# Kernel optimization log

Hardware: AMD Instinct MI355X
Metric: run time of the kernel (lower is better)

Reference implementation:

```python
import jax, jax.numpy as jnp
import numpy as np

B, C, N = 8, 512, 2048
QK, V = 512, 512


def setup_inputs() -> dict:
    key = jax.random.key(0)
    k1, k2, k3, k4 = jax.random.split(key, 4)
    x = jax.random.normal(k1, (B, C, N), dtype=jnp.float32)
    # conv1x1 weights: [out_ch, in_ch]
    w_q = jax.random.normal(k2, (QK, C), dtype=jnp.float32) * (1.0 / np.sqrt(C))
    w_k = w_q  # torch init clones k into q; still independent params
    w_v = jax.random.normal(k3, (V, C), dtype=jnp.float32) * (1.0 / np.sqrt(C))
    b_v = jnp.zeros((V,), dtype=jnp.float32)
    return {"x": x, "w_q": w_q, "w_k": w_k, "w_v": w_v, "b_v": b_v}


def reference(x, w_q, w_k, w_v, b_v):
    temperature = jnp.asarray(w_q.shape[0], x.dtype) ** 0.5
    # conv1x1: [B,C,N] -> [B,out,N]
    q = jnp.einsum('qc,bcn->bnq', w_q, x)            # [B,N,QK]
    k = jnp.einsum('kc,bcn->bkn', w_k, x)            # [B,QK,N]
    v = jnp.einsum('vc,bcn->bnv', w_v, x) + b_v      # [B,N,V]
    energy = jnp.einsum('bnq,bqm->bnm', q, k) / temperature  # [B,N,N]
    attn = jax.nn.softmax(energy, axis=-1)
    out = jnp.einsum('bnm,bmv->bvn', attn, v)        # [B,V,N]
    return out
```

## Files before the change

kernel.cpp:

```cpp
#include <hip/hip_runtime.h>
#include <hip/hip_bf16.h>

#define NBATCH 8
#define CIN 512
#define NLEN 2048
#define DIM 512

typedef __bf16 bf16x8_t __attribute__((ext_vector_type(8)));
typedef __bf16 bf16x4_t __attribute__((ext_vector_type(4)));
typedef float f32x4_t __attribute__((ext_vector_type(4)));
typedef unsigned short ushort4_t __attribute__((ext_vector_type(4)));
typedef unsigned short ushort8_t __attribute__((ext_vector_type(8)));

#define MFMA16(a, b, c) __builtin_amdgcn_mfma_f32_16x16x32_bf16((a), (b), (c), 0, 0, 0)

#define GLOAD_LDS16(g, s)                                                      \
  __builtin_amdgcn_global_load_lds(                                            \
      (const __attribute__((address_space(1))) void*)(g),                      \
      (__attribute__((address_space(3))) void*)(s), 16, 0, 0)

__device__ __forceinline__ unsigned short bfbits(float x) {
  union { __bf16 h; unsigned short u; } c; c.h = (__bf16)x; return c.u;
}
__device__ __forceinline__ ushort4_t pack4(float a, float b, float c, float d) {
  union { bf16x4_t v; ushort4_t u; } u;
  u.v[0] = (__bf16)a; u.v[1] = (__bf16)b; u.v[2] = (__bf16)c; u.v[3] = (__bf16)d;
  return u.u;
}

__global__ void wconv_kernel(const float* __restrict__ wq, const float* __restrict__ wk,
                             const float* __restrict__ wv, unsigned short* __restrict__ wb) {
  int i = (blockIdx.x * 256 + threadIdx.x) * 4;
  const float* s;
  if (i < 262144) s = wq + i;
  else if (i < 524288) s = wk + (i - 262144);
  else s = wv + (i - 524288);
  f32x4_t v = *(const f32x4_t*)s;
  *(ushort4_t*)(wb + i) = pack4(v[0], v[1], v[2], v[3]);
}

__global__ __launch_bounds__(256, 2) void proj_kernel(
    const float* __restrict__ x, const unsigned short* __restrict__ wb,
    const float* __restrict__ bv,
    unsigned short* __restrict__ qb, unsigned short* __restrict__ kb,
    unsigned short* __restrict__ vt, int n_ob) {
  __shared__ __align__(16) unsigned short xt[128][40];
  __shared__ __align__(16) unsigned short wt[128][40];
  __shared__ __align__(16) unsigned short ot[128][132];

  int bid = blockIdx.x;
  int b = bid & 7;
  int j = bid >> 3;
  int n0 = (j & 15) << 7;
  int ob = j >> 4;
  int p = ob >> 2;
  if (n_ob == 8 && p == 1) p = 2;
  int po0 = (ob & 3) << 7;

  const unsigned short* W = wb + p * (DIM * CIN);

  int t = threadIdx.x;
  int w = t >> 6, l = t & 63, lr = l & 15, hi = l >> 4;
  int wr = w >> 1, wc = w & 1;
  int nq = t & 31, cq = t >> 5;
  int wrow = t >> 2, wq4 = t & 3;

  f32x4_t acc[4][4];
#pragma unroll
  for (int rf = 0; rf < 4; ++rf)
#pragma unroll
    for (int cf = 0; cf < 4; ++cf)
      acc[rf][cf] = (f32x4_t){0.f, 0.f, 0.f, 0.f};

  for (int ks = 0; ks < 16; ++ks) {
    int k0 = ks * 32;
    f32x4_t xv[4];
#pragma unroll
    for (int jj = 0; jj < 4; ++jj) {
      int c = k0 + cq * 4 + jj;
      xv[jj] = *(const f32x4_t*)(x + (size_t)(b * CIN + c) * NLEN + n0 + nq * 4);
    }
    bf16x8_t wv8a = *(const bf16x8_t*)(W + (size_t)(po0 + wrow) * CIN + k0 + wq4 * 8);
    bf16x8_t wv8b = *(const bf16x8_t*)(W + (size_t)(po0 + 64 + wrow) * CIN + k0 + wq4 * 8);

    __syncthreads();

#pragma unroll
    for (int i2 = 0; i2 < 4; ++i2)
      *(ushort4_t*)&xt[nq * 4 + i2][cq * 4] =
          pack4(xv[0][i2], xv[1][i2], xv[2][i2], xv[3][i2]);
    *(bf16x8_t*)&wt[wrow][wq4 * 8] = wv8a;
    *(bf16x8_t*)&wt[64 + wrow][wq4 * 8] = wv8b;

    __syncthreads();

    bf16x8_t a4[4], b4[4];
#pragma unroll
    for (int rf = 0; rf < 4; ++rf)
      a4[rf] = *(const bf16x8_t*)&xt[wr * 64 + rf * 16 + lr][hi * 8];
#pragma unroll
    for (int cf = 0; cf < 4; ++cf)
      b4[cf] = *(const bf16x8_t*)&wt[wc * 64 + cf * 16 + lr][hi * 8];

    if (p != 2) {
#pragma unroll
      for (int rf = 0; rf < 4; ++rf)
#pragma unroll
        for (int cf = 0; cf < 4; ++cf)
          acc[rf][cf] = MFMA16(a4[rf], b4[cf], acc[rf][cf]);
    } else {
#pragma unroll
      for (int rf = 0; rf < 4; ++rf)
#pragma unroll
        for (int cf = 0; cf < 4; ++cf)
          acc[rf][cf] = MFMA16(b4[cf], a4[rf], acc[rf][cf]);
    }
  }

  if (p != 2) {
    unsigned short* dst = (p == 0) ? qb : kb;
#pragma unroll
    for (int rf = 0; rf < 4; ++rf)
#pragma unroll
      for (int cf = 0; cf < 4; ++cf) {
        int n = n0 + wr * 64 + rf * 16 + hi * 4;
        int oo = po0 + wc * 64 + cf * 16 + lr;
        unsigned short* d0 = dst + (size_t)(b * NLEN + n) * DIM + oo;
#pragma unroll
        for (int r = 0; r < 4; ++r)
          d0[(size_t)r * DIM] = bfbits(acc[rf][cf][r]);
      }
  } else {
#pragma unroll
    for (int rf = 0; rf < 4; ++rf)
#pragma unroll
      for (int cf = 0; cf < 4; ++cf) {
        int oo_l = wc * 64 + cf * 16 + hi * 4;
        int n_l  = wr * 64 + rf * 16 + lr;
        f32x4_t bb = *(const f32x4_t*)(bv + po0 + oo_l);
        *(ushort4_t*)&ot[n_l][oo_l] =
            pack4(acc[rf][cf][0] + bb[0], acc[rf][cf][1] + bb[1],
                  acc[rf][cf][2] + bb[2], acc[rf][cf][3] + bb[3]);
      }
    __syncthreads();
#pragma unroll
    for (int i = 0; i < 8; ++i) {
      int idx = i * 256 + t;
      int ol = idx & 127, ncl = idx >> 7;
      ushort8_t val;
#pragma unroll
      for (int jj = 0; jj < 8; ++jj) val[jj] = ot[ncl * 8 + jj][ol];
      *(ushort8_t*)(vt + ((size_t)((b * 256 + (n0 >> 3) + ncl) * 512) + po0 + ol) * 8) = val;
    }
  }
}

__global__ __launch_bounds__(512, 2) void attn_kernel(
    const unsigned short* __restrict__ qb, const unsigned short* __restrict__ kb,
    const unsigned short* __restrict__ vc, float* __restrict__ out) {
  __shared__ __align__(16) unsigned short kt[2][64][512];
  __shared__ __align__(16) unsigned short pt[2][4][16][72];
  __shared__ __align__(16) float sclbuf[2][16][4];
  __shared__ __align__(16) float lbuf[16][4];
  __shared__ __align__(16) int flags[2][4];

  int bid = blockIdx.x;
  int b = bid & 7;
  int q0 = (bid >> 3) << 6;
  int t = threadIdx.x;
  int w = t >> 6, l = t & 63, lr = l & 15, hi = l >> 4;
  bool qw = (w < 4);

  const float SCALE2 = 0.0637593663f;

  bf16x8_t qf[16];
  if (qw) {
    const unsigned short* qrow =
        qb + (size_t)(b * NLEN + q0 + w * 16 + lr) * DIM + hi * 8;
#pragma unroll
    for (int cc = 0; cc < 16; ++cc)
      qf[cc] = *(const bf16x8_t*)(qrow + cc * 32);
  }

  f32x4_t oacc[4][4];
#pragma unroll
  for (int qt = 0; qt < 4; ++qt)
#pragma unroll
    for (int vg = 0; vg < 4; ++vg)
      oacc[qt][vg] = (f32x4_t){0.f, 0.f, 0.f, 0.f};

  float m_run = -1e30f, l_lane = 0.f;

  const char* kbase = (const char*)(kb + (size_t)b * NLEN * DIM) + w * 8192;
  const unsigned short* vcb = vc + (size_t)b * NLEN * DIM;
  int l16 = l * 16;

#define STAGE(bi, tt)                                                          \
  do {                                                                         \
    const char* ks = kbase + (size_t)(tt) * 65536;                             \
    _Pragma("unroll")                                                          \
    for (int i = 0; i < 8; ++i)                                                \
      GLOAD_LDS16(ks + i * 1024 + (l16 ^ (i << 4)), &kt[bi][w * 8 + i][0]);    \
  } while (0)

  STAGE(0, 0);
  __syncthreads();

  int rowoff = lr * 1024 + ((hi ^ (lr & 3)) << 4);
  int fsw = (lr & 4) << 4;
  const char* ktbase = (const char*)&kt[0][0][0];

  for (int it = 0; it < 32; ++it) {
    int cur = it & 1;
    if (it < 31) STAGE(cur ^ 1, it + 1);

    bf16x8_t vf[4][2];
#pragma unroll
    for (int vg = 0; vg < 4; ++vg)
#pragma unroll
      for (int ks2 = 0; ks2 < 2; ++ks2)
        vf[vg][ks2] = *(const bf16x8_t*)(vcb +
            ((size_t)(it * 8 + ks2 * 4 + hi) * 512 + w * 64 + vg * 16 + lr) * 8);

    if (qw) {
      const char* kb0 = ktbase + cur * 65536 + rowoff;
      f32x4_t s[4];
#pragma unroll
      for (int j = 0; j < 4; ++j) s[j] = (f32x4_t){0.f, 0.f, 0.f, 0.f};
      __builtin_amdgcn_s_setprio(1);
#pragma unroll
      for (int cc = 0; cc < 16; ++cc) {
        const char* pa = ((cc & 1) ? (kb0 - fsw) : (kb0 + fsw)) + cc * 64;
#pragma unroll
        for (int j = 0; j < 4; ++j) {
          bf16x8_t a0 = *(const bf16x8_t*)(pa + j * 16384);
          s[j] = MFMA16(a0, qf[cc], s[j]);
        }
      }
      __builtin_amdgcn_s_setprio(0);

      float sv[16];
#pragma unroll
      for (int j = 0; j < 4; ++j)
#pragma unroll
        for (int r = 0; r < 4; ++r)
          sv[j * 4 + r] = s[j][r] * SCALE2;
      float tm = sv[0];
#pragma unroll
      for (int i = 1; i < 16; ++i) tm = fmaxf(tm, sv[i]);

      float scl = 1.0f;
      int fl = !__all(tm <= m_run + 20.f);
      if (fl) {
        float gm = fmaxf(tm, __shfl_xor(tm, 16));
        gm = fmaxf(gm, __shfl_xor(gm, 32));
        float mn = fmaxf(m_run, gm);
        scl = exp2f(m_run - mn);
        m_run = mn;
        l_lane *= scl;
      }

      float pex[16];
#pragma unroll
      for (int i = 0; i < 16; ++i) {
        pex[i] = exp2f(sv[i] - m_run);
        l_lane += pex[i];
      }

#pragma unroll
      for (int j = 0; j < 4; ++j)
        *(ushort4_t*)&pt[cur][w][lr][j * 16 + hi * 4] =
            pack4(pex[j * 4], pex[j * 4 + 1], pex[j * 4 + 2], pex[j * 4 + 3]);
      if (hi == 0) sclbuf[cur][lr][w] = scl;
      if (l == 0) flags[cur][w] = fl;
    }

    __syncthreads();

    bf16x8_t pf[4][2];
#pragma unroll
    for (int qt = 0; qt < 4; ++qt)
#pragma unroll
      for (int ks2 = 0; ks2 < 2; ++ks2)
        pf[qt][ks2] = *(const bf16x8_t*)&pt[cur][qt][lr][ks2 * 32 + hi * 8];

    int4 f4 = *(const int4*)&flags[cur][0];
    if (f4.x | f4.y | f4.z | f4.w) {
      f32x4_t s4 = *(const f32x4_t*)&sclbuf[cur][lr][0];
#pragma unroll
      for (int qt = 0; qt < 4; ++qt)
#pragma unroll
        for (int vg = 0; vg < 4; ++vg) {
          oacc[qt][vg][0] *= s4[qt]; oacc[qt][vg][1] *= s4[qt];
          oacc[qt][vg][2] *= s4[qt]; oacc[qt][vg][3] *= s4[qt];
        }
    }

    __builtin_amdgcn_s_setprio(1);
#pragma unroll
    for (int vg = 0; vg < 4; ++vg)
#pragma unroll
      for (int qt = 0; qt < 4; ++qt) {
        oacc[qt][vg] = MFMA16(vf[vg][0], pf[qt][0], oacc[qt][vg]);
        oacc[qt][vg] = MFMA16(vf[vg][1], pf[qt][1], oacc[qt][vg]);
      }
    __builtin_amdgcn_s_setprio(0);
  }

  if (qw) {
    float lt = l_lane + __shfl_xor(l_lane, 16);
    lt += __shfl_xor(lt, 32);
    if (hi == 0) lbuf[lr][w] = lt;
  }
  __syncthreads();
  f32x4_t lv = *(const f32x4_t*)&lbuf[lr][0];
  f32x4_t inv;
#pragma unroll
  for (int qt = 0; qt < 4; ++qt) inv[qt] = 1.0f / lv[qt];

#pragma unroll
  for (int qt = 0; qt < 4; ++qt)
#pragma unroll
    for (int vg = 0; vg < 4; ++vg) {
      int vch = w * 64 + vg * 16 + hi * 4;
      int n = q0 + qt * 16 + lr;
#pragma unroll
      for (int r = 0; r < 4; ++r)
        out[(size_t)(b * DIM + vch + r) * NLEN + n] = oacc[qt][vg][r] * inv[qt];
    }
#undef STAGE
}

extern "C" void kernel_launch(void* const* d_in, const int* in_sizes, int n_in,
                              void* d_out, int out_size, void* d_ws, size_t ws_size,
                              hipStream_t stream) {
  const float* x  = (const float*)d_in[0];
  const float* wq = (const float*)d_in[1];
  const float* wk = (const float*)d_in[2];
  const float* wv = (const float*)d_in[3];
  const float* bv = (const float*)d_in[4];
  float* out = (float*)d_out;

  const size_t ELEMS = (size_t)NBATCH * NLEN * DIM;
  const size_t SZ_PROJ = ELEMS * 2;
  const size_t SZ_W = (size_t)3 * DIM * CIN * 2;
  size_t needA = 3 * SZ_PROJ + SZ_W;

  unsigned short* qb = (unsigned short*)d_ws;
  unsigned short* kb;
  unsigned short* vt;
  unsigned short* wb;
  int n_ob;
  if (ws_size >= needA) {
    kb = qb + ELEMS;
    vt = kb + ELEMS;
    wb = vt + ELEMS;
    n_ob = 12;
  } else {
    kb = qb;
    vt = qb + ELEMS;
    wb = vt + ELEMS;
    n_ob = 8;
  }

  wconv_kernel<<<dim3(768), dim3(256), 0, stream>>>(wq, wk, wv, wb);
  proj_kernel<<<dim3(8 * 16 * n_ob), dim3(256), 0, stream>>>(x, wb, bv, qb, kb, vt, n_ob);
  attn_kernel<<<dim3(256), dim3(512), 0, stream>>>(qb, kb, vt, out);
}
```

Before: 185.3 us.

## Software-pipeline the PV MFMA block one iteration behind the QK/softmax stage

The P·V accumulation for tile it-1 now runs at the start of iteration it, before the QK and softmax work for tile it, instead of after the barrier. The existing double-buffered P, scale and flag buffers are reused, and a final PV block handles the last tile after the loop. The aim is to let warps that do not compute QK do PV work while the QK warps are busy, so the per-tile barrier separates fewer serial phases. In exchange, the V fragments are now loaded from global memory right before their MFMAs rather than being prefetched early, so their load latency may be exposed.

```diff
diff --git a/kernel.cpp b/kernel.cpp
--- a/kernel.cpp
+++ b/kernel.cpp
@@ -203,6 +203,41 @@
       GLOAD_LDS16(ks + i * 1024 + (l16 ^ (i << 4)), &kt[bi][w * 8 + i][0]);    \
   } while (0)
 
+#define PVBLOCK(pb, tprev)                                                     \
+  do {                                                                         \
+    bf16x8_t pf[4][2];                                                         \
+    _Pragma("unroll")                                                          \
+    for (int qt = 0; qt < 4; ++qt)                                             \
+      _Pragma("unroll")                                                        \
+      for (int ks2 = 0; ks2 < 2; ++ks2)                                        \
+        pf[qt][ks2] = *(const bf16x8_t*)&pt[pb][qt][lr][ks2 * 32 + hi * 8];    \
+    int4 f4 = *(const int4*)&flags[pb][0];                                     \
+    if (f4.x | f4.y | f4.z | f4.w) {                                           \
+      f32x4_t s4 = *(const f32x4_t*)&sclbuf[pb][lr][0];                        \
+      _Pragma("unroll")                                                        \
+      for (int qt = 0; qt < 4; ++qt)                                           \
+        _Pragma("unroll")                                                      \
+        for (int vg = 0; vg < 4; ++vg) {                                       \
+          oacc[qt][vg][0] *= s4[qt]; oacc[qt][vg][1] *= s4[qt];                \
+          oacc[qt][vg][2] *= s4[qt]; oacc[qt][vg][3] *= s4[qt];                \
+        }                                                                      \
+    }                                                                          \
+    __builtin_amdgcn_s_setprio(1);                                             \
+    _Pragma("unroll")                                                          \
+    for (int vg = 0; vg < 4; ++vg) {                                           \
+      _Pragma("unroll")                                                        \
+      for (int ks2 = 0; ks2 < 2; ++ks2) {                                      \
+        bf16x8_t vfr = *(const bf16x8_t*)(vcb +                                \
+            ((size_t)((tprev) * 8 + ks2 * 4 + hi) * 512 + w * 64 + vg * 16 +   \
+             lr) * 8);                                                         \
+        _Pragma("unroll")                                                      \
+        for (int qt = 0; qt < 4; ++qt)                                         \
+          oacc[qt][vg] = MFMA16(vfr, pf[qt][ks2], oacc[qt][vg]);               \
+      }                                                                        \
+    }                                                                          \
+    __builtin_amdgcn_s_setprio(0);                                             \
+  } while (0)
+
   STAGE(0, 0);
   __syncthreads();
 
@@ -214,13 +249,7 @@
     int cur = it & 1;
     if (it < 31) STAGE(cur ^ 1, it + 1);
 
-    bf16x8_t vf[4][2];
-#pragma unroll
-    for (int vg = 0; vg < 4; ++vg)
-#pragma unroll
-      for (int ks2 = 0; ks2 < 2; ++ks2)
-        vf[vg][ks2] = *(const bf16x8_t*)(vcb +
-            ((size_t)(it * 8 + ks2 * 4 + hi) * 512 + w * 64 + vg * 16 + lr) * 8);
+    if (it > 0) PVBLOCK(cur ^ 1, it - 1);
 
     if (qw) {
       const char* kb0 = ktbase + cur * 65536 + rowoff;
@@ -276,36 +305,9 @@
     }
 
     __syncthreads();
-
-    bf16x8_t pf[4][2];
-#pragma unroll
-    for (int qt = 0; qt < 4; ++qt)
-#pragma unroll
-      for (int ks2 = 0; ks2 < 2; ++ks2)
-        pf[qt][ks2] = *(const bf16x8_t*)&pt[cur][qt][lr][ks2 * 32 + hi * 8];
-
-    int4 f4 = *(const int4*)&flags[cur][0];
-    if (f4.x | f4.y | f4.z | f4.w) {
-      f32x4_t s4 = *(const f32x4_t*)&sclbuf[cur][lr][0];
-#pragma unroll
-      for (int qt = 0; qt < 4; ++qt)
-#pragma unroll
-        for (int vg = 0; vg < 4; ++vg) {
-          oacc[qt][vg][0] *= s4[qt]; oacc[qt][vg][1] *= s4[qt];
-          oacc[qt][vg][2] *= s4[qt]; oacc[qt][vg][3] *= s4[qt];
-        }
-    }
-
-    __builtin_amdgcn_s_setprio(1);
-#pragma unroll
-    for (int vg = 0; vg < 4; ++vg)
-#pragma unroll
-      for (int qt = 0; qt < 4; ++qt) {
-        oacc[qt][vg] = MFMA16(vf[vg][0], pf[qt][0], oacc[qt][vg]);
-        oacc[qt][vg] = MFMA16(vf[vg][1], pf[qt][1], oacc[qt][vg]);
-      }
-    __builtin_amdgcn_s_setprio(0);
-  }
+  }
+
+  PVBLOCK(1, 31);
 
   if (qw) {
     float lt = l_lane + __shfl_xor(l_lane, 16);
@@ -329,6 +331,7 @@
         out[(size_t)(b * DIM + vch + r) * NLEN + n] = oacc[qt][vg][r] * inv[qt];
     }
 #undef STAGE
+#undef PVBLOCK
 }
 
 extern "C" void kernel_launch(void* const* d_in, const int* in_sizes, int n_in,
```

Measured after the change: 194.7 us. +5.0%, slower.
